# Performance work log

Hardware: AMD Instinct MI355X
Metric: run time of the kernel (lower is better)

The kernel has to match this reference:

```python
import jax, jax.numpy as jnp
import numpy as np

B, T, CIN, HF, G, E = 8, 316, 64, 128, 32, 384
DOWN, MINP, OUT = 2, 8, 8
STRIDE = MINP // DOWN  # finest-grid cell -> feature-map stride


def _build_metas(b, t):
    # Non-overlapping quadtree partition of the 32x32 finest grid:
    # 8x8 macro cells (span 4) all split into span-2 nodes; the first 20 of
    # those are split again into span-1 leaves -> 236 + 80 = 316 tokens.
    # meta row = [tl_row_fg, tl_col_fg, cell_span, patch_px, score]
    span2 = [(r + dr, c + dc) for r in range(0, G, 4) for c in range(0, G, 4)
             for dr in (0, 2) for dc in (0, 2)]
    rows = [[r, c, 2, 16, 0] for (r, c) in span2[20:]]
    rows += [[r + dr, c + dc, 1, 8, 0] for (r, c) in span2[:20]
             for dr in (0, 1) for dc in (0, 1)]
    meta = np.asarray(rows, np.int32)
    rng = np.random.default_rng(0)
    return jnp.asarray(np.stack([meta[rng.permutation(t)] for _ in range(b)], 0))


def setup_inputs():
    key = jax.random.key(0)
    k1, k2 = jax.random.split(key)
    return {
        "x_in": jax.random.normal(k1, (B, CIN, HF, HF), jnp.float32),
        "tokens": jax.random.normal(k2, (B, T, E), jnp.float32),
        "metas": _build_metas(B, T),
    }


def _sample_token(img, r_fg, c_fg, p_px):
    # img: [C, Hf, Wf]. Bilinear resize (align_corners=False, matching
    # F.interpolate) of the [p_feat, p_feat] crop at (r_fg*STRIDE, c_fg*STRIDE)
    # to [OUT, OUT], fully in-place via gathers (no host syncs, no per-token
    # kernel launches).
    p_feat = p_px // DOWN
    pf = jnp.maximum(p_feat, 1).astype(jnp.float32)
    i = jnp.arange(OUT, dtype=jnp.float32)
    rel = jnp.clip((i + 0.5) * (pf / OUT) - 0.5, 0.0, pf - 1.0)
    i0 = jnp.floor(rel)
    w = rel - i0
    i1 = jnp.minimum(i0 + 1.0, pf - 1.0)
    off_r = (r_fg * STRIDE).astype(jnp.float32)
    off_c = (c_fg * STRIDE).astype(jnp.float32)
    y0 = (off_r + i0).astype(jnp.int32); y1 = (off_r + i1).astype(jnp.int32)
    x0 = (off_c + i0).astype(jnp.int32); x1 = (off_c + i1).astype(jnp.int32)
    g = lambda y, x: img[:, y[:, None], x[None, :]]  # [C, OUT, OUT]
    wx = w[None, None, :]; wy = w[None, :, None]
    top = g(y0, x0) * (1 - wx) + g(y0, x1) * wx
    bot = g(y1, x0) * (1 - wx) + g(y1, x1) * wx
    patch = top * (1 - wy) + bot * wy
    return jnp.where(p_px > 0, patch, 0.0)


def _extract_patches(x_in, metas):
    per_img = lambda img, mb: jax.vmap(
        lambda m: _sample_token(img, m[0], m[1], m[3]))(mb)
    return jax.vmap(per_img)(x_in, metas)  # [B, T, C, OUT, OUT]


def _spatial_scatter(tokens, metas):
    # Each token's embedding is tiled over its span x span finest-grid cells.
    # Build an owner-index map via one scatter, then one gather.
    b, t, e = tokens.shape
    r, c, span, p = metas[..., 0], metas[..., 1], metas[..., 2], metas[..., 3]
    di, dj = np.meshgrid(np.arange(4), np.arange(4), indexing="ij")  # max span 4
    di = jnp.asarray(di.reshape(-1)); dj = jnp.asarray(dj.reshape(-1))  # [16]
    rows = r[:, :, None] + di
    cols = c[:, :, None] + dj                                   # [B, T, 16]
    valid = (di < span[:, :, None]) & (dj < span[:, :, None]) & (p[:, :, None] > 0)
    flat = jnp.where(valid, rows * G + cols, G * G)             # dump slot G*G
    owner = jnp.full((b, G * G + 1), -1, jnp.int32)
    b_idx = jnp.arange(b)[:, None, None]
    t_idx = jnp.broadcast_to(jnp.arange(t, dtype=jnp.int32)[None, :, None], flat.shape)
    owner = owner.at[b_idx, flat].set(t_idx)[:, : G * G]        # [B, G*G]
    gathered = jnp.take_along_axis(tokens, jnp.maximum(owner, 0)[:, :, None], axis=1)
    fmap = jnp.where(owner[:, :, None] >= 0, gathered, 0.0)     # [B, G*G, E]
    return fmap.reshape(b, G, G, e).transpose(0, 3, 1, 2)       # [B, E, G, G]


def reference(x_in, tokens, metas):
    patches = _extract_patches(x_in, metas)
    half_span = metas[..., 2].astype(jnp.float32) / 2.0
    cx = metas[..., 1].astype(jnp.float32) + half_span
    cy = metas[..., 0].astype(jnp.float32) + half_span
    p = metas[..., 3]
    scale_idx = jnp.where(p == 16, 1, jnp.where(p == 8, 2, 0)).astype(jnp.int32)
    fmap = _spatial_scatter(tokens, metas)
    return patches, cx, cy, scale_idx, fmap
```

## Files before the change

### kernel.cpp

```cpp
#include <hip/hip_runtime.h>

#define B_      8
#define T_      316
#define CIN_    64
#define HF_     128
#define G_      32
#define E_      384
#define OUT_    8
#define STRIDE_ 4

#define PATCH_SZ  10354688
#define CX_OFF    (PATCH_SZ)
#define CY_OFF    (CX_OFF + B_*T_)
#define SI_OFF    (CY_OFF + B_*T_)
#define FMAP_OFF  (SI_OFF + B_*T_)

__global__ void meta_owner_kernel(const int* __restrict__ metas,
                                  float* __restrict__ out,
                                  int* __restrict__ owner)
{
    const int b   = blockIdx.x;
    const int tid = threadIdx.x;

    __shared__ int own[G_ * G_];
    own[tid] = -1;
    __syncthreads();

    if (tid < T_) {
        const int* m = metas + (b * T_ + tid) * 5;
        const int r = m[0], c = m[1], s = m[2], p = m[3];

        const float hs = (float)s * 0.5f;
        out[CX_OFF + b * T_ + tid] = (float)c + hs;
        out[CY_OFF + b * T_ + tid] = (float)r + hs;
        out[SI_OFF + b * T_ + tid] = (p == 16) ? 1.0f : ((p == 8) ? 2.0f : 0.0f);

        if (p > 0) {
            const int sl = (s < 4) ? s : 4;
            for (int di = 0; di < sl; ++di)
                for (int dj = 0; dj < sl; ++dj) {
                    const int rr = r + di, cc = c + dj;
                    if (rr < G_ && cc < G_)
                        own[rr * G_ + cc] = tid;
                }
        }
    }
    __syncthreads();
    owner[b * G_ * G_ + tid] = own[tid];
}

__global__ void patches_kernel(const float* __restrict__ x,
                               const int* __restrict__ metas,
                               float* __restrict__ out)
{
    const int bt  = blockIdx.x;
    const int b   = bt / T_;
    const int tid = threadIdx.x;

    const int* m = metas + bt * 5;
    const int r = m[0], c = m[1], p = m[3];

    const float* img = x + (size_t)b * CIN_ * HF_ * HF_;
    float*       po  = out + (size_t)bt * CIN_ * OUT_ * OUT_;

    if (p == 16) {
        const float* src = img + (size_t)(r * STRIDE_) * HF_ + c * STRIDE_;
        float4* po4 = (float4*)po;
#pragma unroll
        for (int k = 0; k < 4; ++k) {
            const int u   = tid + k * 256;
            const int ch  = u >> 4;
            const int rem = u & 15;
            const int i   = rem >> 1;
            const int j4  = rem & 1;
            const float4 v = *(const float4*)(src + (size_t)ch * (HF_ * HF_) + i * HF_ + j4 * 4);
            po4[u] = v;
        }
        return;
    }

    const int pix = tid & 63;
    const int i   = pix >> 3;
    const int j   = pix & 7;
    const int ch0 = tid >> 6;

    int pfi = p / 2;
    if (pfi < 1) pfi = 1;
    const float pf    = (float)pfi;
    const float scale = pf * 0.125f;

    const float reli = fminf(fmaxf(((float)i + 0.5f) * scale - 0.5f, 0.0f), pf - 1.0f);
    const float fi0  = floorf(reli);
    const float wy   = reli - fi0;
    const float fi1  = fminf(fi0 + 1.0f, pf - 1.0f);

    const float relj = fminf(fmaxf(((float)j + 0.5f) * scale - 0.5f, 0.0f), pf - 1.0f);
    const float fj0  = floorf(relj);
    const float wx   = relj - fj0;
    const float fj1  = fminf(fj0 + 1.0f, pf - 1.0f);

    const int y0 = r * STRIDE_ + (int)fi0;
    const int y1 = r * STRIDE_ + (int)fi1;
    const int x0 = c * STRIDE_ + (int)fj0;
    const int x1 = c * STRIDE_ + (int)fj1;

    const int r0 = y0 * HF_, r1 = y1 * HF_;

    for (int ch = ch0; ch < CIN_; ch += 4) {
        const float* ip = img + (size_t)ch * (HF_ * HF_);
        const float v00 = ip[r0 + x0];
        const float v01 = ip[r0 + x1];
        const float v10 = ip[r1 + x0];
        const float v11 = ip[r1 + x1];
        const float top = v00 * (1.0f - wx) + v01 * wx;
        const float bot = v10 * (1.0f - wx) + v11 * wx;
        float val       = top * (1.0f - wy) + bot * wy;
        if (p <= 0) val = 0.0f;
        po[ch * (OUT_ * OUT_) + pix] = val;
    }
}

#define EG_ 8
__global__ void fmap_kernel(const float* __restrict__ tokens,
                            const int* __restrict__ owner,
                            float* __restrict__ fmap)
{
    const int b  = blockIdx.x / (E_ / EG_);
    const int eg = blockIdx.x % (E_ / EG_);
    const int t  = threadIdx.x;

    const int4 own = *(const int4*)(owner + b * (G_ * G_) + 4 * t);
    const float* tok = tokens + (size_t)b * T_ * E_ + eg * EG_;
    float4* fm = (float4*)(fmap + (size_t)b * E_ * (G_ * G_) + (size_t)eg * EG_ * (G_ * G_));

#pragma unroll
    for (int e = 0; e < EG_; ++e) {
        float4 v;
        v.x = (own.x >= 0) ? tok[(size_t)own.x * E_ + e] : 0.0f;
        v.y = (own.y >= 0) ? tok[(size_t)own.y * E_ + e] : 0.0f;
        v.z = (own.z >= 0) ? tok[(size_t)own.z * E_ + e] : 0.0f;
        v.w = (own.w >= 0) ? tok[(size_t)own.w * E_ + e] : 0.0f;
        fm[e * 256 + t] = v;
    }
}

extern "C" void kernel_launch(void* const* d_in, const int* in_sizes, int n_in,
                              void* d_out, int out_size, void* d_ws, size_t ws_size,
                              hipStream_t stream) {
    const float* x_in   = (const float*)d_in[0];
    const float* tokens = (const float*)d_in[1];
    const int*   metas  = (const int*)d_in[2];
    float*       out    = (float*)d_out;
    int*         owner  = (int*)d_ws;

    meta_owner_kernel<<<B_, G_ * G_, 0, stream>>>(metas, out, owner);
    patches_kernel<<<B_ * T_, 256, 0, stream>>>(x_in, metas, out);
    fmap_kernel<<<B_ * (E_ / EG_), 256, 0, stream>>>(tokens, owner, out + FMAP_OFF);
}
```

Baseline: 116.4 us.

## Fuse owner, patch and fmap kernels into one launch with per-block owner map

Merges the three kernels into a single launch. The first blocks each rebuild the owner map in shared memory for their batch and write the fmap, and the remaining blocks extract patches. This removes two kernel launches and the global owner round-trip, and lets patch and fmap work run concurrently. The fmap gathers now load 16 contiguous embedding values per owner as float4 vectors instead of scalar loads. The cost is that the owner map is recomputed redundantly in every fmap block (24 per batch), and each thread holds more registers.

```diff
diff --git a/kernel.cpp b/kernel.cpp
--- a/kernel.cpp
+++ b/kernel.cpp
@@ -15,47 +15,85 @@
 #define SI_OFF    (CY_OFF + B_*T_)
 #define FMAP_OFF  (SI_OFF + B_*T_)
 
-__global__ void meta_owner_kernel(const int* __restrict__ metas,
-                                  float* __restrict__ out,
-                                  int* __restrict__ owner)
+#define EG_   16
+#define NF_   (B_ * (E_ / EG_))
+#define NP_   (B_ * T_)
+
+__device__ __forceinline__ void load16(float* d, const float* p, bool ok)
 {
-    const int b   = blockIdx.x;
+    if (ok) {
+        const float4* q = (const float4*)p;
+#pragma unroll
+        for (int k = 0; k < 4; ++k) {
+            const float4 v = q[k];
+            d[4*k+0] = v.x; d[4*k+1] = v.y; d[4*k+2] = v.z; d[4*k+3] = v.w;
+        }
+    } else {
+#pragma unroll
+        for (int k = 0; k < 16; ++k) d[k] = 0.0f;
+    }
+}
+
+__global__ void fused_kernel(const float* __restrict__ x,
+                             const float* __restrict__ tokens,
+                             const int* __restrict__ metas,
+                             float* __restrict__ out)
+{
+    const int blk = blockIdx.x;
     const int tid = threadIdx.x;
 
-    __shared__ int own[G_ * G_];
-    own[tid] = -1;
-    __syncthreads();
+    if (blk < NF_) {
+        const int b  = blk / (E_ / EG_);
+        const int eg = blk % (E_ / EG_);
 
-    if (tid < T_) {
-        const int* m = metas + (b * T_ + tid) * 5;
-        const int r = m[0], c = m[1], s = m[2], p = m[3];
+        __shared__ int own[G_ * G_];
+#pragma unroll
+        for (int k = 0; k < 4; ++k) own[tid + k * 256] = -1;
+        __syncthreads();
 
-        const float hs = (float)s * 0.5f;
-        out[CX_OFF + b * T_ + tid] = (float)c + hs;
-        out[CY_OFF + b * T_ + tid] = (float)r + hs;
-        out[SI_OFF + b * T_ + tid] = (p == 16) ? 1.0f : ((p == 8) ? 2.0f : 0.0f);
+        for (int t = tid; t < T_; t += 256) {
+            const int* m = metas + (b * T_ + t) * 5;
+            const int r = m[0], c = m[1], s = m[2], p = m[3];
 
-        if (p > 0) {
-            const int sl = (s < 4) ? s : 4;
-            for (int di = 0; di < sl; ++di)
-                for (int dj = 0; dj < sl; ++dj) {
-                    const int rr = r + di, cc = c + dj;
-                    if (rr < G_ && cc < G_)
-                        own[rr * G_ + cc] = tid;
-                }
+            if (eg == 0) {
+                const float hs = (float)s * 0.5f;
+                out[CX_OFF + b * T_ + t] = (float)c + hs;
+                out[CY_OFF + b * T_ + t] = (float)r + hs;
+                out[SI_OFF + b * T_ + t] = (p == 16) ? 1.0f : ((p == 8) ? 2.0f : 0.0f);
+            }
+            if (p > 0) {
+                const int sl = (s < 4) ? s : 4;
+                for (int di = 0; di < sl; ++di)
+                    for (int dj = 0; dj < sl; ++dj) {
+                        const int rr = r + di, cc = c + dj;
+                        if (rr < G_ && cc < G_)
+                            own[rr * G_ + cc] = t;
+                    }
+            }
         }
+        __syncthreads();
+
+        const int4 o = *(const int4*)(own + 4 * tid);
+        const float* tok = tokens + (size_t)b * T_ * E_ + eg * EG_;
+
+        float a0[16], a1[16], a2[16], a3[16];
+        load16(a0, tok + (size_t)o.x * E_, o.x >= 0);
+        load16(a1, tok + (size_t)o.y * E_, o.y >= 0);
+        load16(a2, tok + (size_t)o.z * E_, o.z >= 0);
+        load16(a3, tok + (size_t)o.w * E_, o.w >= 0);
+
+        float4* fm = (float4*)(out + FMAP_OFF + (size_t)b * E_ * (G_ * G_)
+                                              + (size_t)eg * EG_ * (G_ * G_));
+#pragma unroll
+        for (int e = 0; e < EG_; ++e) {
+            float4 v; v.x = a0[e]; v.y = a1[e]; v.z = a2[e]; v.w = a3[e];
+            fm[e * 256 + tid] = v;
+        }
+        return;
     }
-    __syncthreads();
-    owner[b * G_ * G_ + tid] = own[tid];
-}
 
-__global__ void patches_kernel(const float* __restrict__ x,
-                               const int* __restrict__ metas,
-                               float* __restrict__ out)
-{
-    const int bt  = blockIdx.x;
-    const int b   = bt / T_;
-    const int tid = threadIdx.x;
+    const int bt = blk - NF_;
+    const int b  = bt / T_;
 
     const int* m = metas + bt * 5;
     const int r = m[0], c = m[1], p = m[3];
@@ -73,8 +111,7 @@
             const int rem = u & 15;
             const int i   = rem >> 1;
             const int j4  = rem & 1;
-            const float4 v = *(const float4*)(src + (size_t)ch * (HF_ * HF_) + i * HF_ + j4 * 4);
-            po4[u] = v;
+            po4[u] = *(const float4*)(src + (size_t)ch * (HF_ * HF_) + i * HF_ + j4 * 4);
         }
         return;
     }
@@ -120,30 +157,6 @@
     }
 }
 
-#define EG_ 8
-__global__ void fmap_kernel(const float* __restrict__ tokens,
-                            const int* __restrict__ owner,
-                            float* __restrict__ fmap)
-{
-    const int b  = blockIdx.x / (E_ / EG_);
-    const int eg = blockIdx.x % (E_ / EG_);
-    const int t  = threadIdx.x;
-
-    const int4 own = *(const int4*)(owner + b * (G_ * G_) + 4 * t);
-    const float* tok = tokens + (size_t)b * T_ * E_ + eg * EG_;
-    float4* fm = (float4*)(fmap + (size_t)b * E_ * (G_ * G_) + (size_t)eg * EG_ * (G_ * G_));
-
-#pragma unroll
-    for (int e = 0; e < EG_; ++e) {
-        float4 v;
-        v.x = (own.x >= 0) ? tok[(size_t)own.x * E_ + e] : 0.0f;
-        v.y = (own.y >= 0) ? tok[(size_t)own.y * E_ + e] : 0.0f;
-        v.z = (own.z >= 0) ? tok[(size_t)own.z * E_ + e] : 0.0f;
-        v.w = (own.w >= 0) ? tok[(size_t)own.w * E_ + e] : 0.0f;
-        fm[e * 256 + t] = v;
-    }
-}
-
 extern "C" void kernel_launch(void* const* d_in, const int* in_sizes, int n_in,
                               void* d_out, int out_size, void* d_ws, size_t ws_size,
                               hipStream_t stream) {
@@ -151,9 +164,6 @@
     const float* tokens = (const float*)d_in[1];
     const int*   metas  = (const int*)d_in[2];
     float*       out    = (float*)d_out;
-    int*         owner  = (int*)d_ws;
 
-    meta_owner_kernel<<<B_, G_ * G_, 0, stream>>>(metas, out, owner);
-    patches_kernel<<<B_ * T_, 256, 0, stream>>>(x_in, metas, out);
-    fmap_kernel<<<B_ * (E_ / EG_), 256, 0, stream>>>(tokens, owner, out + FMAP_OFF);
+    fused_kernel<<<NF_ + NP_, 256, 0, stream>>>(x_in, tokens, metas, out);
 }
```

Result: faster. 106.9 us (-8.2%).
